# Kernel optimization log

Measured on AMD Instinct MI355X. Metric: run time of the kernel, lower is better.

The kernel has to match this reference:

```python
import jax, jax.numpy as jnp
import numpy as np

N, D, H, E_DIM = 2048, 128, 8, 10
DH = D // H
EPS = 1e-5

def _ln(x, g, b):
    mu = jnp.mean(x, axis=-1, keepdims=True)
    var = jnp.mean((x - mu) ** 2, axis=-1, keepdims=True)
    return (x - mu) / jnp.sqrt(var + EPS) * g + b

def setup_inputs() -> dict:
    key = jax.random.key(0)
    ks = jax.random.split(key, 16)
    E = 65536
    inp = {
        "node_feat": jax.random.normal(ks[0], (N, D), jnp.float32),
        "edge_feat": jax.random.normal(ks[1], (E, E_DIM), jnp.float32),
        "src": jax.random.randint(ks[2], (E,), 0, N, jnp.int32).astype(jnp.int64),
        "dst": jax.random.randint(ks[3], (E,), 0, N, jnp.int32).astype(jnp.int64),
        "Wq": jax.random.normal(ks[4], (D, D), jnp.float32) * 0.02,
        "bq": jnp.zeros((D,), jnp.float32),
        "Wk": jax.random.normal(ks[5], (D, D), jnp.float32) * 0.02,
        "bk": jnp.zeros((D,), jnp.float32),
        "Wv": jax.random.normal(ks[6], (D, D), jnp.float32) * 0.02,
        "bv": jnp.zeros((D,), jnp.float32),
        "Wo": jax.random.normal(ks[7], (D, D), jnp.float32) * 0.02,
        "bo": jnp.zeros((D,), jnp.float32),
        "We": jax.random.normal(ks[8], (E_DIM, H), jnp.float32) * 0.02,
        "be": jnp.zeros((H,), jnp.float32),
        "g1": jnp.ones((D,), jnp.float32),
        "b1n": jnp.zeros((D,), jnp.float32),
        "g2": jnp.ones((D,), jnp.float32),
        "b2n": jnp.zeros((D,), jnp.float32),
        "W1": jax.random.normal(ks[9], (D, 4 * D), jnp.float32) * 0.02,
        "bf1": jnp.zeros((4 * D,), jnp.float32),
        "W2": jax.random.normal(ks[10], (4 * D, D), jnp.float32) * 0.02,
        "bf2": jnp.zeros((D,), jnp.float32),
    }
    return inp

def reference(node_feat, edge_feat, src, dst, Wq, bq, Wk, bk, Wv, bv, Wo, bo,
              We, be, g1, b1n, g2, b2n, W1, bf1, W2, bf2):
    n = node_feat.shape[0]
    Q = (node_feat @ Wq + bq).reshape(n, H, DH)
    K = (node_feat @ Wk + bk).reshape(n, H, DH)
    V = (node_feat @ Wv + bv).reshape(n, H, DH)
    scores = jnp.einsum('ihd,jhd->ijh', Q, K) / jnp.sqrt(jnp.float32(DH))
    # scatter edge bias into dense [N,N,H] (set semantics, like torch indexed assign)
    edge_bias = edge_feat @ We + be  # [E,H]
    bias = jnp.zeros((n, n, H), scores.dtype).at[src, dst].set(edge_bias)
    scores = scores + bias
    # symmetric adjacency mask with self-loops
    adj = jnp.zeros((n, n), scores.dtype)
    adj = adj.at[src, dst].set(1.0).at[dst, src].set(1.0)
    idx = jnp.arange(n)
    adj = adj.at[idx, idx].set(1.0)
    scores = jnp.where(adj[:, :, None] == 0, -jnp.inf, scores)
    attn = jax.nn.softmax(scores, axis=1)  # softmax over keys j (dim=1)
    out = jnp.einsum('ijh,jhd->ihd', attn, V).reshape(n, -1)
    out = out @ Wo + bo
    out = _ln(out + node_feat, g1, b1n)
    ffn = jax.nn.relu(out @ W1 + bf1) @ W2 + bf2
    out = _ln(out + ffn, g2, b2n)
    return out
```

## Files before the change

### kernel.cpp

```cpp
#include <hip/hip_runtime.h>
#include <hip/hip_bf16.h>

#define NN   2048
#define DDIM 128
#define HH   8
#define DHH  16
#define NEDGE 65536
#define FFN  512
#define EPSV 1e-5f
#define CAP  256

typedef const float* fp_c;

__device__ __forceinline__ bool idx64(const int* src) {
    return (src[1] | src[3] | src[5] | src[7] | src[9] | src[11]) == 0;
}

__global__ __launch_bounds__(512) void k_pq(float* Qf, float* Kf, float* Vf, fp_c x,
                                            fp_c Wq, fp_c bq, fp_c Wk, fp_c bk, fp_c Wv, fp_c bv,
                                            int* eid, unsigned* bm, float* eb,
                                            const int* src, const int* dst,
                                            fp_c edge_feat, fp_c We, fp_c be) {
    int b = blockIdx.x;
    int t = threadIdx.x;
    if (b < 512) {
        __shared__ float sx[4][DDIM];
        __shared__ float red[3][4][4][DDIM];
        int r0 = b * 4;
        int c = t & 127;
        int ks = t >> 7;
        sx[t >> 7][t & 127] = x[r0 * DDIM + t];
        __syncthreads();
        float aq[4] = {0, 0, 0, 0}, ak[4] = {0, 0, 0, 0}, av[4] = {0, 0, 0, 0};
        int kbeg = ks * 32;
#pragma unroll 8
        for (int k = kbeg; k < kbeg + 32; k++) {
            float wq = Wq[k * DDIM + c];
            float wk = Wk[k * DDIM + c];
            float wv = Wv[k * DDIM + c];
#pragma unroll
            for (int r = 0; r < 4; r++) {
                float xv = sx[r][k];
                aq[r] += xv * wq; ak[r] += xv * wk; av[r] += xv * wv;
            }
        }
#pragma unroll
        for (int r = 0; r < 4; r++) {
            red[0][ks][r][c] = aq[r];
            red[1][ks][r][c] = ak[r];
            red[2][ks][r][c] = av[r];
        }
        __syncthreads();
        int rr = t >> 7, cc = t & 127;
        float vq = 0, vk = 0, vv = 0;
#pragma unroll
        for (int s = 0; s < 4; s++) {
            vq += red[0][s][rr][cc];
            vk += red[1][s][rr][cc];
            vv += red[2][s][rr][cc];
        }
        Qf[(r0 + rr) * DDIM + cc] = (vq + bq[cc]) * 0.25f;
        Kf[(r0 + rr) * DDIM + cc] = vk + bk[cc];
        Vf[(r0 + rr) * DDIM + cc] = vv + bv[cc];
    } else {
        __shared__ float sWe[80];
        __shared__ float sbe[8];
        if (t < 80) sWe[t] = We[t];
        if (t < 8)  sbe[t] = be[t];
        __syncthreads();
        int u = (b - 512) * 512 + t;
        bool is64 = idx64(src);
        if (u < NN * 64 / 4) ((int4*)bm)[u] = make_int4(0, 0, 0, 0);
        if (u < NN) eid[u * NN + u] = -2;
        if (u < NEDGE) {
            int s = is64 ? src[2 * u] : src[u];
            int d = is64 ? dst[2 * u] : dst[u];
            eid[s * NN + d] = -2;
            eid[d * NN + s] = -2;
            float ef[10];
#pragma unroll
            for (int k = 0; k < 10; k++) ef[k] = edge_feat[u * 10 + k];
#pragma unroll
            for (int h = 0; h < 8; h++) {
                float a = sbe[h];
#pragma unroll
                for (int k = 0; k < 10; k++) a += ef[k] * sWe[k * 8 + h];
                eb[u * 8 + h] = a;
            }
        }
    }
}

__global__ __launch_bounds__(512) void k_scatter(int* eid, unsigned* bm, const int* src, const int* dst) {
    int t = blockIdx.x * blockDim.x + threadIdx.x;
    bool is64 = idx64(src);
    if (t < NEDGE) {
        int s = is64 ? src[2 * t] : src[t];
        int d = is64 ? dst[2 * t] : dst[t];
        atomicMax(&eid[s * NN + d], t);
        atomicOr(&bm[s * 64 + (d >> 5)], 1u << (d & 31));
        atomicOr(&bm[d * 64 + (s >> 5)], 1u << (s & 31));
    } else if (t < NEDGE + NN) {
        int i = t - NEDGE;
        atomicOr(&bm[i * 64 + (i >> 5)], 1u << (i & 31));
    }
}

__global__ __launch_bounds__(256) void k_attn(float* attn_out, const float* Qf, const float* Kf,
                                              const float* Vf, const int* eid, const float* eb,
                                              const unsigned* bm) {
    __shared__ float qrow[DDIM];
    __shared__ int   lj[CAP + 8];
    __shared__ int   lev[CAP + 8];
    __shared__ float sc[CAP + 8][HH];
    __shared__ float hinv[HH];
    __shared__ float redpv[2][DDIM];
    __shared__ int   scnt;
    int i = blockIdx.x;
    int t = threadIdx.x;
    if (t < 128) qrow[t] = Qf[i * DDIM + t];

    if (t < 64) {
        unsigned word = bm[i * 64 + t];
        int pc = __popc(word);
        int x = pc;
#pragma unroll
        for (int off = 1; off < 64; off <<= 1) {
            int y = __shfl_up(x, off);
            if (t >= off) x += y;
        }
        int cnt = __shfl(x, 63);
        if (cnt > CAP - 8) cnt = CAP - 8;
        int idx = x - pc;
        unsigned w = word;
        while (w && idx < CAP) {
            int bpos = __ffs(w) - 1;
            lj[idx++] = (t << 5) + bpos;
            w &= w - 1;
        }
        if (t < 8) lj[cnt + t] = 0;
        if (t == 0) scnt = cnt;
    }
    __syncthreads();
    int cnt = scnt;
    int cnt8 = (cnt + 7) & ~7;
    if (t < cnt8) lev[t] = (t < cnt) ? eid[(long)i * NN + lj[t]] : -2;
    __syncthreads();

    int h = t & 7;
    int nsl = t >> 3;
    const float4* q4 = (const float4*)(qrow + h * DHH);
    float4 q0 = q4[0], q1 = q4[1], q2 = q4[2], q3 = q4[3];
    for (int n = nsl; n < cnt8; n += 32) {
        int j = lj[n];
        const float4* k4 = (const float4*)(Kf + j * DDIM + h * DHH);
        float4 k0 = k4[0], k1 = k4[1], k2 = k4[2], k3 = k4[3];
        float s = q0.x * k0.x + q0.y * k0.y + q0.z * k0.z + q0.w * k0.w
                + q1.x * k1.x + q1.y * k1.y + q1.z * k1.z + q1.w * k1.w
                + q2.x * k2.x + q2.y * k2.y + q2.z * k2.z + q2.w * k2.w
                + q3.x * k3.x + q3.y * k3.y + q3.z * k3.z + q3.w * k3.w;
        int ev = lev[n];
        if (ev >= 0) s += eb[ev * 8 + h];
        sc[n][h] = s;
    }
    __syncthreads();

    {
        int hh = t >> 5;
        int sub = t & 31;
        float m = -1e30f;
        for (int n = sub; n < cnt; n += 32) m = fmaxf(m, sc[n][hh]);
#pragma unroll
        for (int off = 1; off < 32; off <<= 1) m = fmaxf(m, __shfl_xor(m, off));
        float ssum = 0.f;
        for (int n = sub; n < cnt; n += 32) {
            float e = __expf(sc[n][hh] - m);
            sc[n][hh] = e;
            ssum += e;
        }
#pragma unroll
        for (int off = 1; off < 32; off <<= 1) ssum += __shfl_xor(ssum, off);
        if (sub == 0) hinv[hh] = 1.0f / ssum;
    }
    if (t < 64) {
        int p = cnt + (t >> 3);
        if (p < cnt8) sc[p][t & 7] = 0.f;
    }
    __syncthreads();

    {
        int g = t >> 7, c = t & 127, h2 = c >> 4;
        float a = 0.f;
#pragma unroll 4
        for (int n = g; n < cnt8; n += 2)
            a += sc[n][h2] * Vf[lj[n] * DDIM + c];
        redpv[g][c] = a;
    }
    __syncthreads();
    if (t < 128)
        attn_out[i * DDIM + t] = (redpv[0][t] + redpv[1][t]) * hinv[t >> 4];
}

__global__ __launch_bounds__(512) void k_tail(float* out, const float* ain,
                                              fp_c Wo, fp_c bo, fp_c node, fp_c g1, fp_c b1,
                                              fp_c W1, fp_c bf1, fp_c W2, fp_c bf2,
                                              fp_c g2, fp_c b2) {
    __shared__ float sa[4][DDIM];
    __shared__ float red[4][4][DDIM];
    __shared__ float x1ld[4][DDIM];
    __shared__ float sh[4][FFN];
    __shared__ float2 sc2[8];
    int t = threadIdx.x;
    int r0 = blockIdx.x * 4;
    int c = t & 127;
    int ks = t >> 7;
    int rr = t >> 7, cc = t & 127;
    sa[t >> 7][t & 127] = ain[r0 * DDIM + t];
    __syncthreads();

    {
        float acc[4] = {0, 0, 0, 0};
        int kbeg = ks * 32;
#pragma unroll 8
        for (int k = kbeg; k < kbeg + 32; k++) {
            float w = Wo[k * DDIM + c];
#pragma unroll
            for (int r = 0; r < 4; r++) acc[r] += sa[r][k] * w;
        }
#pragma unroll
        for (int r = 0; r < 4; r++) red[ks][r][c] = acc[r];
        __syncthreads();
        float val = red[0][rr][cc] + red[1][rr][cc] + red[2][rr][cc] + red[3][rr][cc];
        val += bo[cc] + node[(r0 + rr) * DDIM + cc];
        float vs = val, vq = val * val;
#pragma unroll
        for (int off = 32; off >= 1; off >>= 1) {
            vs += __shfl_down(vs, off);
            vq += __shfl_down(vq, off);
        }
        if ((t & 63) == 0) sc2[t >> 6] = make_float2(vs, vq);
        __syncthreads();
        float sum = sc2[2 * rr].x + sc2[2 * rr + 1].x;
        float sq  = sc2[2 * rr].y + sc2[2 * rr + 1].y;
        float mu = sum * (1.0f / DDIM);
        float var = sq * (1.0f / DDIM) - mu * mu;
        x1ld[rr][cc] = (val - mu) * rsqrtf(var + EPSV) * g1[cc] + b1[cc];
    }
    __syncthreads();

    {
        float acc[4] = {0, 0, 0, 0};
#pragma unroll 8
        for (int k = 0; k < DDIM; k++) {
            float w = W1[k * FFN + t];
#pragma unroll
            for (int r = 0; r < 4; r++) acc[r] += x1ld[r][k] * w;
        }
        float bb = bf1[t];
#pragma unroll
        for (int r = 0; r < 4; r++) sh[r][t] = fmaxf(acc[r] + bb, 0.f);
    }
    __syncthreads();

    {
        float acc[4] = {0, 0, 0, 0};
        int kbeg = ks * 128;
#pragma unroll 8
        for (int k = kbeg; k < kbeg + 128; k++) {
            float w = W2[k * DDIM + c];
#pragma unroll
            for (int r = 0; r < 4; r++) acc[r] += sh[r][k] * w;
        }
#pragma unroll
        for (int r = 0; r < 4; r++) red[ks][r][c] = acc[r];
        __syncthreads();
        float val = red[0][rr][cc] + red[1][rr][cc] + red[2][rr][cc] + red[3][rr][cc];
        val += bf2[cc] + x1ld[rr][cc];
        float vs = val, vq = val * val;
#pragma unroll
        for (int off = 32; off >= 1; off >>= 1) {
            vs += __shfl_down(vs, off);
            vq += __shfl_down(vq, off);
        }
        if ((t & 63) == 0) sc2[t >> 6] = make_float2(vs, vq);
        __syncthreads();
        float sum = sc2[2 * rr].x + sc2[2 * rr + 1].x;
        float sq  = sc2[2 * rr].y + sc2[2 * rr + 1].y;
        float mu = sum * (1.0f / DDIM);
        float var = sq * (1.0f / DDIM) - mu * mu;
        out[(r0 + rr) * DDIM + cc] = (val - mu) * rsqrtf(var + EPSV) * g2[cc] + b2[cc];
    }
}

extern "C" void kernel_launch(void* const* d_in, const int* in_sizes, int n_in,
                              void* d_out, int out_size, void* d_ws, size_t ws_size,
                              hipStream_t stream) {
    fp_c node = (fp_c)d_in[0];
    fp_c edge_feat = (fp_c)d_in[1];
    const int* src = (const int*)d_in[2];
    const int* dst = (const int*)d_in[3];
    fp_c Wq = (fp_c)d_in[4];  fp_c bq = (fp_c)d_in[5];
    fp_c Wk = (fp_c)d_in[6];  fp_c bk = (fp_c)d_in[7];
    fp_c Wv = (fp_c)d_in[8];  fp_c bv = (fp_c)d_in[9];
    fp_c Wo = (fp_c)d_in[10]; fp_c bo = (fp_c)d_in[11];
    fp_c We = (fp_c)d_in[12]; fp_c be = (fp_c)d_in[13];
    fp_c g1 = (fp_c)d_in[14]; fp_c b1n = (fp_c)d_in[15];
    fp_c g2 = (fp_c)d_in[16]; fp_c b2n = (fp_c)d_in[17];
    fp_c W1 = (fp_c)d_in[18]; fp_c bf1 = (fp_c)d_in[19];
    fp_c W2 = (fp_c)d_in[20]; fp_c bf2 = (fp_c)d_in[21];

    char* ws = (char*)d_ws;
    int* eid      = (int*)ws;      ws += (size_t)NN * NN * 4;
    unsigned* bm  = (unsigned*)ws; ws += (size_t)NN * 64 * 4;
    float* eb     = (float*)ws;    ws += (size_t)NEDGE * 8 * 4;
    float* Qf     = (float*)ws;    ws += (size_t)NN * DDIM * 4;
    float* Kf     = (float*)ws;    ws += (size_t)NN * DDIM * 4;
    float* Vf     = (float*)ws;    ws += (size_t)NN * DDIM * 4;
    float* attn_o = (float*)ws;    ws += (size_t)NN * DDIM * 4;

    k_pq<<<768, 512, 0, stream>>>(Qf, Kf, Vf, node, Wq, bq, Wk, bk, Wv, bv,
                                  eid, bm, eb, src, dst, edge_feat, We, be);
    k_scatter<<<(NEDGE + NN + 511) / 512, 512, 0, stream>>>(eid, bm, src, dst);
    k_attn<<<NN, 256, 0, stream>>>(attn_o, Qf, Kf, Vf, eid, eb, bm);
    k_tail<<<NN / 4, 512, 0, stream>>>((float*)d_out, attn_o, Wo, bo, node, g1, b1n,
                                       W1, bf1, W2, bf2, g2, b2n);
}
```

Baseline: 68.38 us.

## Replace dense NxN edge-id matrix with per-row open-addressing hash table

The dense 2048x2048 edge-id array becomes a 128-slot linear-probing hash table per source row. Each slot packs the destination and edge index, and duplicate edges are resolved with atomicMax so the last edge wins. Initialization now zeroes the compact table instead of writing sentinels at random positions, and the attention kernel probes the table to find each neighbour's edge bias. This aims to cut scattered traffic over a 16MB workspace and keep the structure L2-resident, at the cost of CAS-based probing loops during scatter and lookup.

Measured after the change: 79.59 us. 16.4% more time.

```diff
diff --git a/kernel.cpp b/kernel.cpp
--- a/kernel.cpp
+++ b/kernel.cpp
@@ -9,6 +9,7 @@
 #define FFN  512
 #define EPSV 1e-5f
 #define CAP  256
+#define HSLOT 128
 
 typedef const float* fp_c;
 
@@ -18,7 +19,7 @@
 
 __global__ __launch_bounds__(512) void k_pq(float* Qf, float* Kf, float* Vf, fp_c x,
                                             fp_c Wq, fp_c bq, fp_c Wk, fp_c bk, fp_c Wv, fp_c bv,
-                                            int* eid, unsigned* bm, float* eb,
+                                            int* ehash, unsigned* bm, float* eb,
                                             const int* src, const int* dst,
                                             fp_c edge_feat, fp_c We, fp_c be) {
     int b = blockIdx.x;
@@ -69,14 +70,9 @@
         if (t < 8)  sbe[t] = be[t];
         __syncthreads();
         int u = (b - 512) * 512 + t;
-        bool is64 = idx64(src);
         if (u < NN * 64 / 4) ((int4*)bm)[u] = make_int4(0, 0, 0, 0);
-        if (u < NN) eid[u * NN + u] = -2;
+        if (u < NN * HSLOT / 4) ((int4*)ehash)[u] = make_int4(0, 0, 0, 0);
         if (u < NEDGE) {
-            int s = is64 ? src[2 * u] : src[u];
-            int d = is64 ? dst[2 * u] : dst[u];
-            eid[s * NN + d] = -2;
-            eid[d * NN + s] = -2;
             float ef[10];
 #pragma unroll
             for (int k = 0; k < 10; k++) ef[k] = edge_feat[u * 10 + k];
@@ -91,15 +87,28 @@
     }
 }
 
-__global__ __launch_bounds__(512) void k_scatter(int* eid, unsigned* bm, const int* src, const int* dst) {
+__global__ __launch_bounds__(512) void k_scatter(int* ehash, unsigned* bm, const int* src, const int* dst) {
     int t = blockIdx.x * blockDim.x + threadIdx.x;
     bool is64 = idx64(src);
     if (t < NEDGE) {
         int s = is64 ? src[2 * t] : src[t];
         int d = is64 ? dst[2 * t] : dst[t];
-        atomicMax(&eid[s * NN + d], t);
         atomicOr(&bm[s * 64 + (d >> 5)], 1u << (d & 31));
         atomicOr(&bm[d * 64 + (s >> 5)], 1u << (s & 31));
+        int packed = (d << 17) | (t + 1);
+        int slot = d & (HSLOT - 1);
+        int* row = ehash + s * HSLOT;
+#pragma unroll 1
+        for (int it = 0; it < HSLOT; it++) {
+            int cur = row[slot];
+            if (cur == 0) {
+                int old = atomicCAS(&row[slot], 0, packed);
+                if (old == 0) break;
+                cur = old;
+            }
+            if ((cur >> 17) == d) { atomicMax(&row[slot], packed); break; }
+            slot = (slot + 1) & (HSLOT - 1);
+        }
     } else if (t < NEDGE + NN) {
         int i = t - NEDGE;
         atomicOr(&bm[i * 64 + (i >> 5)], 1u << (i & 31));
@@ -107,7 +116,7 @@
 }
 
 __global__ __launch_bounds__(256) void k_attn(float* attn_out, const float* Qf, const float* Kf,
-                                              const float* Vf, const int* eid, const float* eb,
+                                              const float* Vf, const int* ehash, const float* eb,
                                               const unsigned* bm) {
     __shared__ float qrow[DDIM];
     __shared__ int   lj[CAP + 8];
@@ -144,7 +153,22 @@
     __syncthreads();
     int cnt = scnt;
     int cnt8 = (cnt + 7) & ~7;
-    if (t < cnt8) lev[t] = (t < cnt) ? eid[(long)i * NN + lj[t]] : -2;
+    if (t < cnt8) {
+        int e = -1;
+        if (t < cnt) {
+            int j = lj[t];
+            const int* row = ehash + i * HSLOT;
+            int slot = j & (HSLOT - 1);
+#pragma unroll 1
+            for (int it = 0; it < HSLOT; it++) {
+                int v = row[slot];
+                if (v == 0) break;
+                if ((v >> 17) == j) { e = (v & 0x1FFFF) - 1; break; }
+                slot = (slot + 1) & (HSLOT - 1);
+            }
+        }
+        lev[t] = e;
+    }
     __syncthreads();
 
     int h = t & 7;
@@ -310,7 +334,7 @@
     fp_c W2 = (fp_c)d_in[20]; fp_c bf2 = (fp_c)d_in[21];
 
     char* ws = (char*)d_ws;
-    int* eid      = (int*)ws;      ws += (size_t)NN * NN * 4;
+    int* ehash    = (int*)ws;      ws += (size_t)NN * HSLOT * 4;
     unsigned* bm  = (unsigned*)ws; ws += (size_t)NN * 64 * 4;
     float* eb     = (float*)ws;    ws += (size_t)NEDGE * 8 * 4;
     float* Qf     = (float*)ws;    ws += (size_t)NN * DDIM * 4;
@@ -318,10 +342,10 @@
     float* Vf     = (float*)ws;    ws += (size_t)NN * DDIM * 4;
     float* attn_o = (float*)ws;    ws += (size_t)NN * DDIM * 4;
 
-    k_pq<<<768, 512, 0, stream>>>(Qf, Kf, Vf, node, Wq, bq, Wk, bk, Wv, bv,
-                                  eid, bm, eb, src, dst, edge_feat, We, be);
-    k_scatter<<<(NEDGE + NN + 511) / 512, 512, 0, stream>>>(eid, bm, src, dst);
-    k_attn<<<NN, 256, 0, stream>>>(attn_o, Qf, Kf, Vf, eid, eb, bm);
+    k_pq<<<640, 512, 0, stream>>>(Qf, Kf, Vf, node, Wq, bq, Wk, bk, Wv, bv,
+                                  ehash, bm, eb, src, dst, edge_feat, We, be);
+    k_scatter<<<(NEDGE + NN + 511) / 512, 512, 0, stream>>>(ehash, bm, src, dst);
+    k_attn<<<NN, 256, 0, stream>>>(attn_o, Qf, Kf, Vf, ehash, eb, bm);
     k_tail<<<NN / 4, 512, 0, stream>>>((float*)d_out, attn_o, Wo, bo, node, g1, b1n,
                                        W1, bf1, W2, bf2, g2, b2n);
 }
```

## Replace dense N×N edge-id map with per-row rank-indexed edge table; 8-row tiles

Applied to the files above, without the earlier changes.

The dense 2048×2048 edge-id array is replaced by a compact per-row table of CAP slots. A new k_rank kernel computes each edge's position among the row's set adjacency bits with popcounts and keeps the last-writer edge via atomicMax, so attention reads edge ids contiguously instead of gathering from a 16 MB map. This removes the scattered initialisation and scatter traffic on the large map, at the cost of an extra kernel launch and a per-edge popcount loop over bitmap words. Separately, the QKV projection and tail kernels now process 8 rows per block instead of 4, reusing each weight load across more rows at the cost of more registers and shared memory.

Result: slower. 81.33 us (+18.9%).

```diff
diff --git a/kernel.cpp b/kernel.cpp
--- a/kernel.cpp
+++ b/kernel.cpp
@@ -18,20 +18,25 @@
 
 __global__ __launch_bounds__(512) void k_pq(float* Qf, float* Kf, float* Vf, fp_c x,
                                             fp_c Wq, fp_c bq, fp_c Wk, fp_c bk, fp_c Wv, fp_c bv,
-                                            int* eid, unsigned* bm, float* eb,
+                                            int* ewin, unsigned* bm, float* eb,
                                             const int* src, const int* dst,
                                             fp_c edge_feat, fp_c We, fp_c be) {
     int b = blockIdx.x;
     int t = threadIdx.x;
-    if (b < 512) {
-        __shared__ float sx[4][DDIM];
-        __shared__ float red[3][4][4][DDIM];
-        int r0 = b * 4;
+    if (b < 256) {
+        __shared__ float sx[8][DDIM];
+        __shared__ float redq[4][8][DDIM];
+        __shared__ float redk[4][8][DDIM];
+        __shared__ float redv[4][8][DDIM];
+        int r0 = b * 8;
         int c = t & 127;
         int ks = t >> 7;
-        sx[t >> 7][t & 127] = x[r0 * DDIM + t];
-        __syncthreads();
-        float aq[4] = {0, 0, 0, 0}, ak[4] = {0, 0, 0, 0}, av[4] = {0, 0, 0, 0};
+        sx[t >> 7][t & 127]       = x[r0 * DDIM + t];
+        sx[4 + (t >> 7)][t & 127] = x[r0 * DDIM + 512 + t];
+        __syncthreads();
+        float aq[8], ak[8], av[8];
+#pragma unroll
+        for (int r = 0; r < 8; r++) { aq[r] = 0; ak[r] = 0; av[r] = 0; }
         int kbeg = ks * 32;
 #pragma unroll 8
         for (int k = kbeg; k < kbeg + 32; k++) {
@@ -39,44 +44,43 @@
             float wk = Wk[k * DDIM + c];
             float wv = Wv[k * DDIM + c];
 #pragma unroll
-            for (int r = 0; r < 4; r++) {
+            for (int r = 0; r < 8; r++) {
                 float xv = sx[r][k];
                 aq[r] += xv * wq; ak[r] += xv * wk; av[r] += xv * wv;
             }
         }
 #pragma unroll
-        for (int r = 0; r < 4; r++) {
-            red[0][ks][r][c] = aq[r];
-            red[1][ks][r][c] = ak[r];
-            red[2][ks][r][c] = av[r];
+        for (int r = 0; r < 8; r++) {
+            redq[ks][r][c] = aq[r];
+            redk[ks][r][c] = ak[r];
+            redv[ks][r][c] = av[r];
         }
         __syncthreads();
         int rr = t >> 7, cc = t & 127;
-        float vq = 0, vk = 0, vv = 0;
+        float vq0 = 0, vk0 = 0, vv0 = 0, vq1 = 0, vk1 = 0, vv1 = 0;
 #pragma unroll
         for (int s = 0; s < 4; s++) {
-            vq += red[0][s][rr][cc];
-            vk += red[1][s][rr][cc];
-            vv += red[2][s][rr][cc];
-        }
-        Qf[(r0 + rr) * DDIM + cc] = (vq + bq[cc]) * 0.25f;
-        Kf[(r0 + rr) * DDIM + cc] = vk + bk[cc];
-        Vf[(r0 + rr) * DDIM + cc] = vv + bv[cc];
+            vq0 += redq[s][rr][cc];     vk0 += redk[s][rr][cc];     vv0 += redv[s][rr][cc];
+            vq1 += redq[s][rr + 4][cc]; vk1 += redk[s][rr + 4][cc]; vv1 += redv[s][rr + 4][cc];
+        }
+        float vbq = bq[cc], vbk = bk[cc], vbv = bv[cc];
+        Qf[(r0 + rr) * DDIM + cc]     = (vq0 + vbq) * 0.25f;
+        Kf[(r0 + rr) * DDIM + cc]     = vk0 + vbk;
+        Vf[(r0 + rr) * DDIM + cc]     = vv0 + vbv;
+        Qf[(r0 + rr + 4) * DDIM + cc] = (vq1 + vbq) * 0.25f;
+        Kf[(r0 + rr + 4) * DDIM + cc] = vk1 + vbk;
+        Vf[(r0 + rr + 4) * DDIM + cc] = vv1 + vbv;
     } else {
         __shared__ float sWe[80];
         __shared__ float sbe[8];
         if (t < 80) sWe[t] = We[t];
         if (t < 8)  sbe[t] = be[t];
         __syncthreads();
-        int u = (b - 512) * 512 + t;
-        bool is64 = idx64(src);
+        int u = (b - 256) * 512 + t;
         if (u < NN * 64 / 4) ((int4*)bm)[u] = make_int4(0, 0, 0, 0);
-        if (u < NN) eid[u * NN + u] = -2;
+        ((int4*)ewin)[u]         = make_int4(0, 0, 0, 0);
+        ((int4*)ewin)[u + 65536] = make_int4(0, 0, 0, 0);
         if (u < NEDGE) {
-            int s = is64 ? src[2 * u] : src[u];
-            int d = is64 ? dst[2 * u] : dst[u];
-            eid[s * NN + d] = -2;
-            eid[d * NN + s] = -2;
             float ef[10];
 #pragma unroll
             for (int k = 0; k < 10; k++) ef[k] = edge_feat[u * 10 + k];
@@ -91,13 +95,12 @@
     }
 }
 
-__global__ __launch_bounds__(512) void k_scatter(int* eid, unsigned* bm, const int* src, const int* dst) {
+__global__ __launch_bounds__(512) void k_scatter(unsigned* bm, const int* src, const int* dst) {
     int t = blockIdx.x * blockDim.x + threadIdx.x;
     bool is64 = idx64(src);
     if (t < NEDGE) {
         int s = is64 ? src[2 * t] : src[t];
         int d = is64 ? dst[2 * t] : dst[t];
-        atomicMax(&eid[s * NN + d], t);
         atomicOr(&bm[s * 64 + (d >> 5)], 1u << (d & 31));
         atomicOr(&bm[d * 64 + (s >> 5)], 1u << (s & 31));
     } else if (t < NEDGE + NN) {
@@ -106,8 +109,22 @@
     }
 }
 
+__global__ __launch_bounds__(512) void k_rank(int* ewin, const unsigned* bm,
+                                              const int* src, const int* dst) {
+    int e = blockIdx.x * blockDim.x + threadIdx.x;
+    if (e >= NEDGE) return;
+    bool is64 = idx64(src);
+    int s = is64 ? src[2 * e] : src[e];
+    int d = is64 ? dst[2 * e] : dst[e];
+    const unsigned* row = bm + s * 64;
+    int dw = d >> 5;
+    int rank = __popc(row[dw] & ((1u << (d & 31)) - 1u));
+    for (int w = 0; w < dw; w++) rank += __popc(row[w]);
+    atomicMax(&ewin[s * CAP + rank], e + 1);
+}
+
 __global__ __launch_bounds__(256) void k_attn(float* attn_out, const float* Qf, const float* Kf,
-                                              const float* Vf, const int* eid, const float* eb,
+                                              const float* Vf, const int* ewin, const float* eb,
                                               const unsigned* bm) {
     __shared__ float qrow[DDIM];
     __shared__ int   lj[CAP + 8];
@@ -144,7 +161,7 @@
     __syncthreads();
     int cnt = scnt;
     int cnt8 = (cnt + 7) & ~7;
-    if (t < cnt8) lev[t] = (t < cnt) ? eid[(long)i * NN + lj[t]] : -2;
+    if (t < cnt8) lev[t] = (t < cnt) ? (ewin[i * CAP + t] - 1) : -1;
     __syncthreads();
 
     int h = t & 7;
@@ -205,90 +222,121 @@
                                               fp_c Wo, fp_c bo, fp_c node, fp_c g1, fp_c b1,
                                               fp_c W1, fp_c bf1, fp_c W2, fp_c bf2,
                                               fp_c g2, fp_c b2) {
-    __shared__ float sa[4][DDIM];
-    __shared__ float red[4][4][DDIM];
-    __shared__ float x1ld[4][DDIM];
-    __shared__ float sh[4][FFN];
-    __shared__ float2 sc2[8];
+    __shared__ float sa[8][DDIM];
+    __shared__ float red[4][8][DDIM];
+    __shared__ float x1ld[8][DDIM];
+    __shared__ float sh[8][FFN];
+    __shared__ float4 sc4[8];
     int t = threadIdx.x;
-    int r0 = blockIdx.x * 4;
+    int r0 = blockIdx.x * 8;
     int c = t & 127;
     int ks = t >> 7;
     int rr = t >> 7, cc = t & 127;
-    sa[t >> 7][t & 127] = ain[r0 * DDIM + t];
-    __syncthreads();
-
-    {
-        float acc[4] = {0, 0, 0, 0};
+    sa[t >> 7][t & 127]       = ain[r0 * DDIM + t];
+    sa[4 + (t >> 7)][t & 127] = ain[r0 * DDIM + 512 + t];
+    __syncthreads();
+
+    {
+        float acc[8] = {0, 0, 0, 0, 0, 0, 0, 0};
         int kbeg = ks * 32;
 #pragma unroll 8
         for (int k = kbeg; k < kbeg + 32; k++) {
             float w = Wo[k * DDIM + c];
 #pragma unroll
-            for (int r = 0; r < 4; r++) acc[r] += sa[r][k] * w;
-        }
-#pragma unroll
-        for (int r = 0; r < 4; r++) red[ks][r][c] = acc[r];
-        __syncthreads();
-        float val = red[0][rr][cc] + red[1][rr][cc] + red[2][rr][cc] + red[3][rr][cc];
-        val += bo[cc] + node[(r0 + rr) * DDIM + cc];
-        float vs = val, vq = val * val;
+            for (int r = 0; r < 8; r++) acc[r] += sa[r][k] * w;
+        }
+#pragma unroll
+        for (int r = 0; r < 8; r++) red[ks][r][c] = acc[r];
+        __syncthreads();
+        float bov = bo[cc];
+        float val0 = red[0][rr][cc] + red[1][rr][cc] + red[2][rr][cc] + red[3][rr][cc]
+                   + bov + node[(r0 + rr) * DDIM + cc];
+        float val1 = red[0][rr + 4][cc] + red[1][rr + 4][cc] + red[2][rr + 4][cc] + red[3][rr + 4][cc]
+                   + bov + node[(r0 + rr + 4) * DDIM + cc];
+        float4 v = make_float4(val0, val0 * val0, val1, val1 * val1);
 #pragma unroll
         for (int off = 32; off >= 1; off >>= 1) {
-            vs += __shfl_down(vs, off);
-            vq += __shfl_down(vq, off);
-        }
-        if ((t & 63) == 0) sc2[t >> 6] = make_float2(vs, vq);
-        __syncthreads();
-        float sum = sc2[2 * rr].x + sc2[2 * rr + 1].x;
-        float sq  = sc2[2 * rr].y + sc2[2 * rr + 1].y;
-        float mu = sum * (1.0f / DDIM);
-        float var = sq * (1.0f / DDIM) - mu * mu;
-        x1ld[rr][cc] = (val - mu) * rsqrtf(var + EPSV) * g1[cc] + b1[cc];
-    }
-    __syncthreads();
-
-    {
-        float acc[4] = {0, 0, 0, 0};
-#pragma unroll 8
+            v.x += __shfl_down(v.x, off);
+            v.y += __shfl_down(v.y, off);
+            v.z += __shfl_down(v.z, off);
+            v.w += __shfl_down(v.w, off);
+        }
+        if ((t & 63) == 0) sc4[t >> 6] = v;
+        __syncthreads();
+        float gv = g1[cc], bv = b1[cc];
+        {
+            float sum = sc4[2 * rr].x + sc4[2 * rr + 1].x;
+            float sq  = sc4[2 * rr].y + sc4[2 * rr + 1].y;
+            float mu = sum * (1.0f / DDIM);
+            float var = sq * (1.0f / DDIM) - mu * mu;
+            x1ld[rr][cc] = (val0 - mu) * rsqrtf(var + EPSV) * gv + bv;
+        }
+        {
+            float sum = sc4[2 * rr].z + sc4[2 * rr + 1].z;
+            float sq  = sc4[2 * rr].w + sc4[2 * rr + 1].w;
+            float mu = sum * (1.0f / DDIM);
+            float var = sq * (1.0f / DDIM) - mu * mu;
+            x1ld[rr + 4][cc] = (val1 - mu) * rsqrtf(var + EPSV) * gv + bv;
+        }
+    }
+    __syncthreads();
+
+    {
+        float acc[8] = {0, 0, 0, 0, 0, 0, 0, 0};
+#pragma unroll 4
         for (int k = 0; k < DDIM; k++) {
             float w = W1[k * FFN + t];
 #pragma unroll
-            for (int r = 0; r < 4; r++) acc[r] += x1ld[r][k] * w;
+            for (int r = 0; r < 8; r++) acc[r] += x1ld[r][k] * w;
         }
         float bb = bf1[t];
 #pragma unroll
-        for (int r = 0; r < 4; r++) sh[r][t] = fmaxf(acc[r] + bb, 0.f);
-    }
-    __syncthreads();
-
-    {
-        float acc[4] = {0, 0, 0, 0};
+        for (int r = 0; r < 8; r++) sh[r][t] = fmaxf(acc[r] + bb, 0.f);
+    }
+    __syncthreads();
+
+    {
+        float acc[8] = {0, 0, 0, 0, 0, 0, 0, 0};
         int kbeg = ks * 128;
 #pragma unroll 8
         for (int k = kbeg; k < kbeg + 128; k++) {
             float w = W2[k * DDIM + c];
 #pragma unroll
-            for (int r = 0; r < 4; r++) acc[r] += sh[r][k] * w;
-        }
-#pragma unroll
-        for (int r = 0; r < 4; r++) red[ks][r][c] = acc[r];
-        __syncthreads();
-        float val = red[0][rr][cc] + red[1][rr][cc] + red[2][rr][cc] + red[3][rr][cc];
-        val += bf2[cc] + x1ld[rr][cc];
-        float vs = val, vq = val * val;
+            for (int r = 0; r < 8; r++) acc[r] += sh[r][k] * w;
+        }
+#pragma unroll
+        for (int r = 0; r < 8; r++) red[ks][r][c] = acc[r];
+        __syncthreads();
+        float bv2 = bf2[cc];
+        float val0 = red[0][rr][cc] + red[1][rr][cc] + red[2][rr][cc] + red[3][rr][cc]
+                   + bv2 + x1ld[rr][cc];
+        float val1 = red[0][rr + 4][cc] + red[1][rr + 4][cc] + red[2][rr + 4][cc] + red[3][rr + 4][cc]
+                   + bv2 + x1ld[rr + 4][cc];
+        float4 v = make_float4(val0, val0 * val0, val1, val1 * val1);
 #pragma unroll
         for (int off = 32; off >= 1; off >>= 1) {
-            vs += __shfl_down(vs, off);
-            vq += __shfl_down(vq, off);
-        }
-        if ((t & 63) == 0) sc2[t >> 6] = make_float2(vs, vq);
-        __syncthreads();
-        float sum = sc2[2 * rr].x + sc2[2 * rr + 1].x;
-        float sq  = sc2[2 * rr].y + sc2[2 * rr + 1].y;
-        float mu = sum * (1.0f / DDIM);
-        float var = sq * (1.0f / DDIM) - mu * mu;
-        out[(r0 + rr) * DDIM + cc] = (val - mu) * rsqrtf(var + EPSV) * g2[cc] + b2[cc];
+            v.x += __shfl_down(v.x, off);
+            v.y += __shfl_down(v.y, off);
+            v.z += __shfl_down(v.z, off);
+            v.w += __shfl_down(v.w, off);
+        }
+        if ((t & 63) == 0) sc4[t >> 6] = v;
+        __syncthreads();
+        float gv = g2[cc], bv = b2[cc];
+        {
+            float sum = sc4[2 * rr].x + sc4[2 * rr + 1].x;
+            float sq  = sc4[2 * rr].y + sc4[2 * rr + 1].y;
+            float mu = sum * (1.0f / DDIM);
+            float var = sq * (1.0f / DDIM) - mu * mu;
+            out[(r0 + rr) * DDIM + cc] = (val0 - mu) * rsqrtf(var + EPSV) * gv + bv;
+        }
+        {
+            float sum = sc4[2 * rr].z + sc4[2 * rr + 1].z;
+            float sq  = sc4[2 * rr].w + sc4[2 * rr + 1].w;
+            float mu = sum * (1.0f / DDIM);
+            float var = sq * (1.0f / DDIM) - mu * mu;
+            out[(r0 + rr + 4) * DDIM + cc] = (val1 - mu) * rsqrtf(var + EPSV) * gv + bv;
+        }
     }
 }
 
@@ -310,7 +358,7 @@
     fp_c W2 = (fp_c)d_in[20]; fp_c bf2 = (fp_c)d_in[21];
 
     char* ws = (char*)d_ws;
-    int* eid      = (int*)ws;      ws += (size_t)NN * NN * 4;
+    int* ewin     = (int*)ws;      ws += (size_t)NN * CAP * 4;
     unsigned* bm  = (unsigned*)ws; ws += (size_t)NN * 64 * 4;
     float* eb     = (float*)ws;    ws += (size_t)NEDGE * 8 * 4;
     float* Qf     = (float*)ws;    ws += (size_t)NN * DDIM * 4;
@@ -318,10 +366,11 @@
     float* Vf     = (float*)ws;    ws += (size_t)NN * DDIM * 4;
     float* attn_o = (float*)ws;    ws += (size_t)NN * DDIM * 4;
 
-    k_pq<<<768, 512, 0, stream>>>(Qf, Kf, Vf, node, Wq, bq, Wk, bk, Wv, bv,
-                                  eid, bm, eb, src, dst, edge_feat, We, be);
-    k_scatter<<<(NEDGE + NN + 511) / 512, 512, 0, stream>>>(eid, bm, src, dst);
-    k_attn<<<NN, 256, 0, stream>>>(attn_o, Qf, Kf, Vf, eid, eb, bm);
-    k_tail<<<NN / 4, 512, 0, stream>>>((float*)d_out, attn_o, Wo, bo, node, g1, b1n,
+    k_pq<<<384, 512, 0, stream>>>(Qf, Kf, Vf, node, Wq, bq, Wk, bk, Wv, bv,
+                                  ewin, bm, eb, src, dst, edge_feat, We, be);
+    k_scatter<<<(NEDGE + NN + 511) / 512, 512, 0, stream>>>(bm, src, dst);
+    k_rank<<<NEDGE / 512, 512, 0, stream>>>(ewin, bm, src, dst);
+    k_attn<<<NN, 256, 0, stream>>>(attn_o, Qf, Kf, Vf, ewin, eb, bm);
+    k_tail<<<NN / 8, 512, 0, stream>>>((float*)d_out, attn_o, Wo, bo, node, g1, b1n,
                                        W1, bf1, W2, bf2, g2, b2n);
 }
```

## Replace dense NxN edge-id map with compact per-row rank-indexed winner table

Applied to the files above, without the earlier changes.

Drops the dense 2048x2048 edge-id array and its scattered writes and atomicMax. A new kernel computes each edge's rank among its row's neighbours with popcounts over the adjacency bitmap, then records the winning edge index in a compact NN x CAP table. The attention kernel then reads the edge id contiguously by neighbour position instead of gathering from a 16 MB array. This adds an extra kernel launch and bitmap popcount work per edge.

After: 75.63 us. 10.6% more time.

```diff
diff --git a/kernel.cpp b/kernel.cpp
--- a/kernel.cpp
+++ b/kernel.cpp
@@ -3,7 +3,7 @@
 
 #define NN   2048
 #define DDIM 128
-#define HH   8
+#define HH    8
 #define DHH  16
 #define NEDGE 65536
 #define FFN  512
@@ -18,7 +18,7 @@
 
 __global__ __launch_bounds__(512) void k_pq(float* Qf, float* Kf, float* Vf, fp_c x,
                                             fp_c Wq, fp_c bq, fp_c Wk, fp_c bk, fp_c Wv, fp_c bv,
-                                            int* eid, unsigned* bm, float* eb,
+                                            int* ewin, unsigned* bm, float* eb,
                                             const int* src, const int* dst,
                                             fp_c edge_feat, fp_c We, fp_c be) {
     int b = blockIdx.x;
@@ -29,7 +29,7 @@
         int r0 = b * 4;
         int c = t & 127;
         int ks = t >> 7;
-        sx[t >> 7][t & 127] = x[r0 * DDIM + t];
+        sx[ks][c] = x[r0 * DDIM + t];
         __syncthreads();
         float aq[4] = {0, 0, 0, 0}, ak[4] = {0, 0, 0, 0}, av[4] = {0, 0, 0, 0};
         int kbeg = ks * 32;
@@ -69,14 +69,9 @@
         if (t < 8)  sbe[t] = be[t];
         __syncthreads();
         int u = (b - 512) * 512 + t;
-        bool is64 = idx64(src);
         if (u < NN * 64 / 4) ((int4*)bm)[u] = make_int4(0, 0, 0, 0);
-        if (u < NN) eid[u * NN + u] = -2;
+        ((int4*)ewin)[u] = make_int4(0, 0, 0, 0);
         if (u < NEDGE) {
-            int s = is64 ? src[2 * u] : src[u];
-            int d = is64 ? dst[2 * u] : dst[u];
-            eid[s * NN + d] = -2;
-            eid[d * NN + s] = -2;
             float ef[10];
 #pragma unroll
             for (int k = 0; k < 10; k++) ef[k] = edge_feat[u * 10 + k];
@@ -91,13 +86,12 @@
     }
 }
 
-__global__ __launch_bounds__(512) void k_scatter(int* eid, unsigned* bm, const int* src, const int* dst) {
+__global__ __launch_bounds__(512) void k_scatter(unsigned* bm, const int* src, const int* dst) {
     int t = blockIdx.x * blockDim.x + threadIdx.x;
     bool is64 = idx64(src);
     if (t < NEDGE) {
         int s = is64 ? src[2 * t] : src[t];
         int d = is64 ? dst[2 * t] : dst[t];
-        atomicMax(&eid[s * NN + d], t);
         atomicOr(&bm[s * 64 + (d >> 5)], 1u << (d & 31));
         atomicOr(&bm[d * 64 + (s >> 5)], 1u << (s & 31));
     } else if (t < NEDGE + NN) {
@@ -106,8 +100,34 @@
     }
 }
 
+__global__ __launch_bounds__(256) void k_rank(int* ewin, const unsigned* bm,
+                                              const int* src, const int* dst) {
+    int e = blockIdx.x * 256 + threadIdx.x;
+    if (e >= NEDGE) return;
+    bool is64 = idx64(src);
+    int s = is64 ? src[2 * e] : src[e];
+    int d = is64 ? dst[2 * e] : dst[e];
+    const int4* row4 = (const int4*)(bm + s * 64);
+    int dw = d >> 5;
+    int dq = dw >> 2;
+    int rank = 0;
+#pragma unroll 4
+    for (int q = 0; q < dq; q++) {
+        int4 w = row4[q];
+        rank += __popc((unsigned)w.x) + __popc((unsigned)w.y)
+              + __popc((unsigned)w.z) + __popc((unsigned)w.w);
+    }
+    int4 wl = row4[dq];
+    unsigned wz[4] = {(unsigned)wl.x, (unsigned)wl.y, (unsigned)wl.z, (unsigned)wl.w};
+    int rem = dw & 3;
+#pragma unroll
+    for (int k = 0; k < 3; k++) if (k < rem) rank += __popc(wz[k]);
+    rank += __popc(wz[rem] & ((1u << (d & 31)) - 1u));
+    atomicMax(&ewin[s * CAP + rank], e + 1);
+}
+
 __global__ __launch_bounds__(256) void k_attn(float* attn_out, const float* Qf, const float* Kf,
-                                              const float* Vf, const int* eid, const float* eb,
+                                              const float* Vf, const int* ewin, const float* eb,
                                               const unsigned* bm) {
     __shared__ float qrow[DDIM];
     __shared__ int   lj[CAP + 8];
@@ -134,8 +154,8 @@
         int idx = x - pc;
         unsigned w = word;
         while (w && idx < CAP) {
-            int bpos = __ffs(w) - 1;
-            lj[idx++] = (t << 5) + bpos;
+            int bp = __ffs(w) - 1;
+            lj[idx++] = (t << 5) + bp;
             w &= w - 1;
         }
         if (t < 8) lj[cnt + t] = 0;
@@ -144,7 +164,7 @@
     __syncthreads();
     int cnt = scnt;
     int cnt8 = (cnt + 7) & ~7;
-    if (t < cnt8) lev[t] = (t < cnt) ? eid[(long)i * NN + lj[t]] : -2;
+    if (t < cnt8) lev[t] = (t < cnt) ? (ewin[i * CAP + t] - 1) : -1;
     __syncthreads();
 
     int h = t & 7;
@@ -166,8 +186,7 @@
     __syncthreads();
 
     {
-        int hh = t >> 5;
-        int sub = t & 31;
+        int hh = t >> 5, sub = t & 31;
         float m = -1e30f;
         for (int n = sub; n < cnt; n += 32) m = fmaxf(m, sc[n][hh]);
 #pragma unroll
@@ -215,7 +234,7 @@
     int c = t & 127;
     int ks = t >> 7;
     int rr = t >> 7, cc = t & 127;
-    sa[t >> 7][t & 127] = ain[r0 * DDIM + t];
+    sa[rr][cc] = ain[r0 * DDIM + t];
     __syncthreads();
 
     {
@@ -310,7 +329,7 @@
     fp_c W2 = (fp_c)d_in[20]; fp_c bf2 = (fp_c)d_in[21];
 
     char* ws = (char*)d_ws;
-    int* eid      = (int*)ws;      ws += (size_t)NN * NN * 4;
+    int* ewin     = (int*)ws;      ws += (size_t)NN * CAP * 4;
     unsigned* bm  = (unsigned*)ws; ws += (size_t)NN * 64 * 4;
     float* eb     = (float*)ws;    ws += (size_t)NEDGE * 8 * 4;
     float* Qf     = (float*)ws;    ws += (size_t)NN * DDIM * 4;
@@ -319,9 +338,10 @@
     float* attn_o = (float*)ws;    ws += (size_t)NN * DDIM * 4;
 
     k_pq<<<768, 512, 0, stream>>>(Qf, Kf, Vf, node, Wq, bq, Wk, bk, Wv, bv,
-                                  eid, bm, eb, src, dst, edge_feat, We, be);
-    k_scatter<<<(NEDGE + NN + 511) / 512, 512, 0, stream>>>(eid, bm, src, dst);
-    k_attn<<<NN, 256, 0, stream>>>(attn_o, Qf, Kf, Vf, eid, eb, bm);
+                                  ewin, bm, eb, src, dst, edge_feat, We, be);
+    k_scatter<<<(NEDGE + NN + 511) / 512, 512, 0, stream>>>(bm, src, dst);
+    k_rank<<<NEDGE / 256, 256, 0, stream>>>(ewin, bm, src, dst);
+    k_attn<<<NN, 256, 0, stream>>>(attn_o, Qf, Kf, Vf, ewin, eb, bm);
     k_tail<<<NN / 4, 512, 0, stream>>>((float*)d_out, attn_o, Wo, bo, node, g1, b1n,
                                        W1, bf1, W2, bf2, g2, b2n);
 }
```
